# Kernel tuning notes

Hardware: AMD Instinct MI355X
Metric: run time of the kernel (lower is better)

Reference implementation:

```python
import jax, jax.numpy as jnp
import numpy as np

DEPTH = 6
IN_DIM = 768
NODE_HIDDEN = 16
LEAF_HIDDEN = 128
OUT_DIM = 768
BATCH = 4096
N_NODES = 2 ** DEPTH - 1   # 63 gating MLPs (heap/BFS order, root first)
N_LEAVES = 2 ** DEPTH      # 64 leaf MLPs


def setup_inputs() -> dict:
    key = jax.random.key(0)
    ks = jax.random.split(key, 5)
    def winit(k, shape, fan_in):
        return jax.random.normal(k, shape, jnp.float32) * (1.0 / np.sqrt(fan_in))
    return {
        "x": jax.random.normal(ks[0], (BATCH, IN_DIM), jnp.float32),
        "node_w1": winit(ks[1], (N_NODES, IN_DIM, NODE_HIDDEN), IN_DIM),
        "node_b1": jnp.zeros((N_NODES, NODE_HIDDEN), jnp.float32),
        "node_w2": winit(ks[2], (N_NODES, NODE_HIDDEN, 1), NODE_HIDDEN),
        "node_b2": jnp.zeros((N_NODES, 1), jnp.float32),
        "leaf_w1": winit(ks[3], (N_LEAVES, IN_DIM, LEAF_HIDDEN), IN_DIM),
        "leaf_b1": jnp.zeros((N_LEAVES, LEAF_HIDDEN), jnp.float32),
        "leaf_w2": winit(ks[4], (N_LEAVES, LEAF_HIDDEN, OUT_DIM), LEAF_HIDDEN),
        "leaf_b2": jnp.zeros((N_LEAVES, OUT_DIM), jnp.float32),
    }


def reference(x, node_w1, node_b1, node_w2, node_b2,
              leaf_w1, leaf_b1, leaf_w2, leaf_b2):
    """Training-mode (soft-gating) FFF tree, fully batched over all nodes/leaves.

    Equivalent to the recursive torch forward with training=True and the
    stochastic output-swap disabled (swap is a training-noise trick).
    """
    B = x.shape[0]
    # All node gates in one pass: c[b, n] = sigmoid(W2 @ relu(W1 @ x + b1) + b2)
    hn = jax.nn.relu(jnp.einsum('bi,nih->bnh', x, node_w1) + node_b1)
    c = jax.nn.sigmoid(jnp.einsum('bnh,nho->bno', hn, node_w2) + node_b2)[..., 0]  # [B, N_NODES]
    # All leaf MLPs in one pass (identity out activation)
    hl = jax.nn.relu(jnp.einsum('bi,lih->blh', x, leaf_w1) + leaf_b1)             # [B, L, LEAF_HIDDEN]
    y = jnp.einsum('blh,lho->blo', hl, leaf_w2) + leaf_b2                         # [B, L, OUT]
    # Leaf mixture weights: product of c (left) / (1-c) (right) along root->leaf path.
    # Heap index idx has children 2*idx, 2*idx+1; gate c weights the LEFT child.
    w = jnp.ones((B, 1), x.dtype)
    for lvl in range(DEPTH):
        g = c[:, 2 ** lvl - 1: 2 ** (lvl + 1) - 1]        # gates at this level, [B, 2^lvl]
        w = jnp.stack([w * g, w * (1.0 - g)], axis=-1).reshape(B, 2 ** (lvl + 1))
    return jnp.einsum('bl,blo->bo', w, y)                 # [B, OUT]
```

## Files before the change

kernel.cpp:

```cpp
#include <hip/hip_runtime.h>
#include <stdint.h>
#include <stddef.h>

typedef __attribute__((ext_vector_type(8))) short short8;
typedef __attribute__((ext_vector_type(4))) float f32x4;
typedef __attribute__((ext_vector_type(4))) short short4v;

__device__ __forceinline__ short f2bf(float f) {
  unsigned u = __builtin_bit_cast(unsigned, f);
  u = (u + 0x7fffu + ((u >> 16) & 1u)) >> 16;
  return (short)u;
}

__device__ __forceinline__ void gload16(const void* g, void* l) {
  __builtin_amdgcn_global_load_lds(
      (const __attribute__((address_space(1))) unsigned int*)g,
      (__attribute__((address_space(3))) unsigned int*)l, 16, 0, 0);
}


__global__ __launch_bounds__(256)
void cvt_misc_k(const float* __restrict__ x, const float* __restrict__ nw1,
                const float* __restrict__ lb2, short* __restrict__ xb,
                short* __restrict__ BTn, short* __restrict__ BT2) {
  const int bx = blockIdx.x;
  if (bx < 3072) {
    const int i = bx * 256 + threadIdx.x;
    const float4 v = ((const float4*)x)[i];
    short4v o;
    o.x = f2bf(v.x); o.y = f2bf(v.y); o.z = f2bf(v.z); o.w = f2bf(v.w);
    *(short4v*)(xb + (size_t)i * 4) = o;
  } else if (bx < 6144) {
    const int idx = (bx - 3072) * 256 + threadIdx.x;
    const int i = idx % 768;
    const int nh = idx / 768;
    float v = 0.f;
    if (nh < 1008) v = nw1[((size_t)(nh >> 4) * 768 + i) * 16 + (nh & 15)];
    BTn[idx] = f2bf(v);
  } else {
    const int idx = (bx - 6144) * 256 + threadIdx.x;
    const int o = idx >> 6, l = idx & 63;
    BT2[(size_t)o * 8256 + 8192 + l] = f2bf(lb2[(size_t)l * 768 + o]);
  }
}

__global__ __launch_bounds__(256, 4)
void node_cvt_k(const short* __restrict__ xb, const short* __restrict__ BTn,
                float* __restrict__ hn, const float* __restrict__ lw1,
                const float* __restrict__ lw2, short* __restrict__ BT1,
                short* __restrict__ BT2) {
  __shared__ char sh[24576];
  const int tid = threadIdx.x;
  if (blockIdx.x < 512) {
    constexpr int ABYTES = 64 * 128;
    const int lane = tid & 63, wid = tid >> 6;
    const int wm = wid >> 1, wn = wid & 1;
    const int sid = (blockIdx.x & 7) * 64 + (blockIdx.x >> 3);
    const int xg = sid % 8, yg = sid / 8;
    const int m0 = yg * 64, n0 = xg * 128;
    f32x4 acc[2][4];
    const f32x4 zero = {0.f, 0.f, 0.f, 0.f};
#pragma unroll
    for (int i = 0; i < 2; ++i)
#pragma unroll
      for (int j = 0; j < 4; ++j) acc[i][j] = zero;
    for (int ki = 0; ki < 12; ++ki) {
      const int k0 = ki * 64;
      __syncthreads();
#pragma unroll
      for (int s = 0; s < 6; ++s) {
        const int off = s * 4096 + tid * 16;
        const short* src;
        if (off < ABYTES) {
          const int r = off >> 7;
          const int cs = ((off >> 4) & 7) ^ (r & 7);
          src = xb + (size_t)(m0 + r) * 768 + k0 + cs * 8;
        } else {
          const int o2 = off - ABYTES;
          const int r = o2 >> 7;
          const int cs = ((o2 >> 4) & 7) ^ (r & 7);
          src = BTn + (size_t)(n0 + r) * 768 + k0 + cs * 8;
        }
        gload16(src, sh + off);
      }
      __syncthreads();
#pragma unroll
      for (int kk = 0; kk < 2; ++kk) {
        const int chunk = kk * 4 + (lane >> 4);
        short8 af[2], bfr[4];
#pragma unroll
        for (int i = 0; i < 2; ++i) {
          const int row = wm * 32 + i * 16 + (lane & 15);
          af[i] = *(const short8*)(sh + row * 128 + ((chunk ^ (row & 7)) << 4));
        }
#pragma unroll
        for (int j = 0; j < 4; ++j) {
          const int row = wn * 64 + j * 16 + (lane & 15);
          bfr[j] = *(const short8*)(sh + ABYTES + row * 128 + ((chunk ^ (row & 7)) << 4));
        }
#pragma unroll
        for (int i = 0; i < 2; ++i)
#pragma unroll
          for (int j = 0; j < 4; ++j)
            acc[i][j] = __builtin_amdgcn_mfma_f32_16x16x32_bf16(af[i], bfr[j], acc[i][j], 0, 0, 0);
      }
    }
    const int row_base = m0 + wm * 32 + (lane >> 4) * 4;
    const int col_base = n0 + wn * 64 + (lane & 15);
#pragma unroll
    for (int i = 0; i < 2; ++i)
#pragma unroll
      for (int j = 0; j < 4; ++j)
#pragma unroll
        for (int r = 0; r < 4; ++r)
          hn[(size_t)(row_base + i * 16 + r) * 1024 + col_base + j * 16] = acc[i][j][r];
  } else {
    float (*tile)[65] = (float(*)[65])sh;
    const int cb = blockIdx.x - 512;
    const int z = cb / 24, rem = cb % 24;
    const int by = rem / 12, bxx = rem % 12;
    const int h0 = by * 64, i0 = bxx * 64;
    if (z < 64) {
      const int l = z;
#pragma unroll
      for (int t = 0; t < 16; ++t) {
        const int e = t * 256 + tid;
        const int ii = e >> 6, hh = e & 63;
        tile[ii][hh] = lw1[(size_t)l * 98304 + (size_t)(i0 + ii) * 128 + (h0 + hh)];
      }
      __syncthreads();
#pragma unroll
      for (int t = 0; t < 16; ++t) {
        const int e = t * 256 + tid;
        const int hh = e >> 6, ii = e & 63;
        BT1[(size_t)(l * 128 + h0 + hh) * 768 + i0 + ii] = f2bf(tile[ii][hh]);
      }
    } else {
      const int l = z - 64;
      const int o0 = i0;
#pragma unroll
      for (int t = 0; t < 16; ++t) {
        const int e = t * 256 + tid;
        const int hh = e >> 6, oo = e & 63;
        tile[hh][oo] = lw2[(size_t)l * 98304 + (size_t)(h0 + hh) * 768 + (o0 + oo)];
      }
      __syncthreads();
#pragma unroll
      for (int t = 0; t < 16; ++t) {
        const int e = t * 256 + tid;
        const int oo = e >> 6, hh = e & 63;
        BT2[(size_t)(o0 + oo) * 8256 + l * 128 + h0 + hh] = f2bf(tile[hh][oo]);
      }
    }
  }
}

__global__ __launch_bounds__(256)
void gates_k(const float* __restrict__ hn, const float* __restrict__ nb1,
             const float* __restrict__ nw2, const float* __restrict__ nb2,
             float* __restrict__ wgt, short* __restrict__ hs) {
  const int b = blockIdx.x * 4 + (threadIdx.x >> 6);
  const int lane = threadIdx.x & 63;
  float c = 0.f;
  if (lane < 63) {
    float s = nb2[lane];
    const float* h = hn + (size_t)b * 1024 + lane * 16;
#pragma unroll
    for (int j = 0; j < 16; ++j) {
      float v = fmaxf(h[j] + nb1[lane * 16 + j], 0.f);
      s += v * nw2[lane * 16 + j];
    }
    c = 1.f / (1.f + expf(-s));
  }
  float w = 1.f;
#pragma unroll
  for (int lvl = 0; lvl < 6; ++lvl) {
    const int idx = (1 << lvl) - 1 + (lane >> (6 - lvl));
    const float g = __shfl(c, idx, 64);
    w *= ((lane >> (5 - lvl)) & 1) ? (1.f - g) : g;
  }
  wgt[(size_t)b * 64 + lane] = w;
  hs[(size_t)b * 8256 + 8192 + lane] = f2bf(w);
}

template <int EPI>
__global__ __launch_bounds__(512, 2)
void gemm8x(const short* __restrict__ A, const short* __restrict__ B,
            void* __restrict__ C0, float* __restrict__ P1, float* __restrict__ P2,
            float* __restrict__ P3, const float* __restrict__ bias,
            const float* __restrict__ wgt) {
  constexpr int LDA = EPI ? 768 : 8256;
  constexpr int LDB = EPI ? 768 : 8256;
  constexpr int LDC = EPI ? 8256 : 768;
  constexpr int ABYTES = 256 * 128;
  constexpr int TILEB = 2 * ABYTES;
  __shared__ char lds[2 * TILEB];

  const int tid = threadIdx.x, lane = tid & 63, wid = tid >> 6;
  const int wm = wid >> 2, wn = wid & 3;

  const int c = blockIdx.x & 7, ii = blockIdx.x >> 3;
  int xg, yg, kt0, ktn, zz;
  if constexpr (EPI == 1) {
    xg = ((c & 3) << 3) + (ii & 7);
    yg = ((c >> 2) << 3) + (ii >> 3);
    kt0 = 0; ktn = 12; zz = 0;
  } else {
    xg = ii % 3;
    const int yz = c * 8 + ii / 3;
    yg = yz & 15;
    zz = yz >> 4;
    kt0 = zz * 32;
    ktn = (zz == 3) ? 33 : 32;
  }
  const int m0 = yg * 256, n0 = xg * 256;

  f32x4 acc[8][4];
  const f32x4 zero = {0.f, 0.f, 0.f, 0.f};
#pragma unroll
  for (int i = 0; i < 8; ++i)
#pragma unroll
    for (int j = 0; j < 4; ++j) acc[i][j] = zero;

  auto STG = [&](int buf, int mat, int h, int kt) {
    const int k0 = kt * 64;
    char* dst = lds + buf * TILEB + mat * ABYTES + h * 16384;
    const short* base = mat ? B : A;
    const int ld = mat ? LDB : LDA;
    const int r0 = (mat ? n0 : m0) + h * 128;
#pragma unroll
    for (int s = 0; s < 2; ++s) {
      const int off = s * 8192 + tid * 16;
      const int r = off >> 7;
      const int cs = ((off >> 4) & 7) ^ (r & 7);
      gload16(base + (size_t)(r0 + r) * ld + k0 + cs * 8, dst + off);
    }
  };

  short8 bfrag[4][2];
  auto RD_B = [&](int buf) {
    const char* bB = lds + buf * TILEB + ABYTES;
#pragma unroll
    for (int j = 0; j < 4; ++j)
#pragma unroll
      for (int kk = 0; kk < 2; ++kk) {
        const int row = wn * 64 + j * 16 + (lane & 15);
        const int chunk = kk * 4 + (lane >> 4);
        bfrag[j][kk] = *(const short8*)(bB + row * 128 + ((chunk ^ (row & 7)) << 4));
      }
  };

  auto PH = [&](int buf, int q, bool rdB, int vm, auto&& stages) {
    if (rdB) RD_B(buf);
    const char* bA = lds + buf * TILEB;
    short8 af[2][2];
#pragma unroll
    for (int i = 0; i < 2; ++i)
#pragma unroll
      for (int kk = 0; kk < 2; ++kk) {
        const int row = wm * 128 + q * 32 + i * 16 + (lane & 15);
        const int chunk = kk * 4 + (lane >> 4);
        af[i][kk] = *(const short8*)(bA + row * 128 + ((chunk ^ (row & 7)) << 4));
      }
    stages();
    if (vm == 4) asm volatile("s_waitcnt vmcnt(4)" ::: "memory");
    else if (vm == 0) asm volatile("s_waitcnt vmcnt(0)" ::: "memory");
    __builtin_amdgcn_s_barrier();
    __builtin_amdgcn_s_setprio(1);
#pragma unroll
    for (int kk = 0; kk < 2; ++kk)
#pragma unroll
      for (int i = 0; i < 2; ++i)
#pragma unroll
        for (int j = 0; j < 4; ++j)
          acc[q * 2 + i][j] =
              __builtin_amdgcn_mfma_f32_16x16x32_bf16(af[i][kk], bfrag[j][kk], acc[q * 2 + i][j], 0, 0, 0);
    __builtin_amdgcn_s_setprio(0);
    __builtin_amdgcn_s_barrier();
  };

  STG(0, 0, 0, kt0); STG(0, 0, 1, kt0); STG(0, 1, 0, kt0); STG(0, 1, 1, kt0);
  STG(1, 1, 0, kt0 + 1); STG(1, 1, 1, kt0 + 1);
  asm volatile("s_waitcnt vmcnt(4)" ::: "memory");
  __builtin_amdgcn_s_barrier();

  const int iters = ktn >> 1;
  for (int it = 0; it < iters; ++it) {
    const int t0 = it * 2;
    const bool lastp = (it == iters - 1) && !(ktn & 1);
    const bool t2 = t0 + 2 < ktn, t3 = t0 + 3 < ktn;
    PH(0, 0, true, -1, [&] { STG(1, 0, 0, kt0 + t0 + 1); });
    PH(0, 1, false, -1, [&] {
      STG(1, 0, 1, kt0 + t0 + 1);
      if (t2) STG(0, 1, 0, kt0 + t0 + 2);
    });
    PH(0, 2, false, -1, [&] { if (t2) STG(0, 1, 1, kt0 + t0 + 2); });
    PH(0, 3, false, lastp ? 0 : 4, [] {});
    PH(1, 0, true, -1, [&] { if (t2) STG(0, 0, 0, kt0 + t0 + 2); });
    PH(1, 1, false, -1, [&] { if (t2) STG(0, 0, 1, kt0 + t0 + 2); });
    PH(1, 2, false, -1, [&] { if (t3) STG(1, 1, 0, kt0 + t0 + 3); });
    PH(1, 3, false, lastp ? -1 : 4, [&] { if (t3) STG(1, 1, 1, kt0 + t0 + 3); });
  }
  if (ktn & 1) {
    asm volatile("s_waitcnt vmcnt(0)" ::: "memory");
    __builtin_amdgcn_s_barrier();
    RD_B(0);
    const char* bA = lds;
#pragma unroll
    for (int q = 0; q < 4; ++q) {
      short8 af[2][2];
#pragma unroll
      for (int i = 0; i < 2; ++i)
#pragma unroll
        for (int kk = 0; kk < 2; ++kk) {
          const int row = wm * 128 + q * 32 + i * 16 + (lane & 15);
          const int chunk = kk * 4 + (lane >> 4);
          af[i][kk] = *(const short8*)(bA + row * 128 + ((chunk ^ (row & 7)) << 4));
        }
      __builtin_amdgcn_s_setprio(1);
#pragma unroll
      for (int kk = 0; kk < 2; ++kk)
#pragma unroll
        for (int i = 0; i < 2; ++i)
#pragma unroll
          for (int j = 0; j < 4; ++j)
            acc[q * 2 + i][j] =
                __builtin_amdgcn_mfma_f32_16x16x32_bf16(af[i][kk], bfrag[j][kk], acc[q * 2 + i][j], 0, 0, 0);
      __builtin_amdgcn_s_setprio(0);
    }
  }

  if constexpr (EPI == 1) {
    short* C = (short*)C0;
#pragma unroll
    for (int mi = 0; mi < 8; ++mi) {
      const int row_base = m0 + wm * 128 + mi * 16 + (lane >> 4) * 4;
#pragma unroll
      for (int j = 0; j < 4; ++j) {
        const int col = n0 + wn * 64 + j * 16 + (lane & 15);
        const int leaf = col >> 7;
        const float b = bias[col];
#pragma unroll
        for (int r = 0; r < 4; ++r) {
          const int row = row_base + r;
          const float v = fmaxf(acc[mi][j][r] + b, 0.f) * wgt[(size_t)row * 64 + leaf];
          C[(size_t)row * LDC + col] = f2bf(v);
        }
      }
    }
  } else {
    float* C = (zz == 0) ? (float*)C0 : (zz == 1 ? P1 : (zz == 2 ? P2 : P3));
#pragma unroll
    for (int mi = 0; mi < 8; ++mi) {
      const int row_base = m0 + wm * 128 + mi * 16 + (lane >> 4) * 4;
#pragma unroll
      for (int j = 0; j < 4; ++j) {
        const int col = n0 + wn * 64 + j * 16 + (lane & 15);
#pragma unroll
        for (int r = 0; r < 4; ++r) {
          const int row = row_base + r;
          C[(size_t)row * LDC + col] = acc[mi][j][r];
        }
      }
    }
  }
}

__global__ __launch_bounds__(256)
void reduce_k(float* __restrict__ out, const float* __restrict__ p1,
              const float* __restrict__ p2, const float* __restrict__ p3) {
  const int i = blockIdx.x * 256 + threadIdx.x;
  f32x4 a = ((const f32x4*)out)[i];
  f32x4 b = ((const f32x4*)p1)[i];
  f32x4 c = ((const f32x4*)p2)[i];
  f32x4 d = ((const f32x4*)p3)[i];
  ((f32x4*)out)[i] = (a + b) + (c + d);
}


extern "C" void kernel_launch(void* const* d_in, const int* in_sizes, int n_in,
                              void* d_out, int out_size, void* d_ws, size_t ws_size,
                              hipStream_t stream) {
  const float* x   = (const float*)d_in[0];
  const float* nw1 = (const float*)d_in[1];
  const float* nb1 = (const float*)d_in[2];
  const float* nw2 = (const float*)d_in[3];
  const float* nb2 = (const float*)d_in[4];
  const float* lw1 = (const float*)d_in[5];
  const float* lb1 = (const float*)d_in[6];
  const float* lw2 = (const float*)d_in[7];
  const float* lb2 = (const float*)d_in[8];

  char* ws = (char*)d_ws;
  short* xb  = (short*)(ws + 0);
  short* BT1 = (short*)(ws + 6291456);
  short* BTn = (short*)(ws + 18874368);
  float* hn  = (float*)(ws + 20447232);
  float* wgt = (float*)(ws + 37224448);
  short* BT2 = (short*)(ws + 38273024);
  short* hs  = (short*)(ws + 50954240);
  float* p1  = (float*)(ws + 0);
  float* p2  = (float*)(ws + 12582912);
  float* p3  = (float*)(ws + 25165824);

  cvt_misc_k<<<6336, 256, 0, stream>>>(x, nw1, lb2, xb, BTn, BT2);
  node_cvt_k<<<3584, 256, 0, stream>>>(xb, BTn, hn, lw1, lw2, BT1, BT2);

  gates_k<<<1024, 256, 0, stream>>>(hn, nb1, nw2, nb2, wgt, hs);

  gemm8x<1><<<512, 512, 0, stream>>>(xb, BT1, hs, nullptr, nullptr, nullptr,
                                     lb1, wgt);

  gemm8x<0><<<192, 512, 0, stream>>>(hs, BT2, d_out, p1, p2, p3,
                                     nullptr, nullptr);

  reduce_k<<<3072, 256, 0, stream>>>((float*)d_out, p1, p2, p3);
}
```

Measured before the change: 161.1 us.

## Rebalance GEMM grids: two N-tiles per block in GEMM1, 5-way split-K in GEMM2

The first GEMM now gives each block two adjacent 256-wide N tiles, processed back to back with a mid-loop epilogue flush. This halves the grid to 256 blocks, so a 256-CU part fills in one wave with a continuous pipeline. The second GEMM moves from 4-way to 5-way split-K (240 blocks) to fill the device better, and stores two of the partials in bf16 to cut write and reduce traffic. The cost is lower precision in part of the output accumulation and more reduction partials.

```diff
diff --git a/kernel.cpp b/kernel.cpp
--- a/kernel.cpp
+++ b/kernel.cpp
@@ -10,6 +10,11 @@
   unsigned u = __builtin_bit_cast(unsigned, f);
   u = (u + 0x7fffu + ((u >> 16) & 1u)) >> 16;
   return (short)u;
+}
+
+__device__ __forceinline__ float bf2f(short s) {
+  unsigned u = ((unsigned)(unsigned short)s) << 16;
+  return __builtin_bit_cast(float, u);
 }
 
 __device__ __forceinline__ void gload16(const void* g, void* l) {
@@ -187,8 +192,8 @@
 __global__ __launch_bounds__(512, 2)
 void gemm8x(const short* __restrict__ A, const short* __restrict__ B,
             void* __restrict__ C0, float* __restrict__ P1, float* __restrict__ P2,
-            float* __restrict__ P3, const float* __restrict__ bias,
-            const float* __restrict__ wgt) {
+            short* __restrict__ Q1, short* __restrict__ Q2,
+            const float* __restrict__ bias, const float* __restrict__ wgt) {
   constexpr int LDA = EPI ? 768 : 8256;
   constexpr int LDB = EPI ? 768 : 8256;
   constexpr int LDC = EPI ? 8256 : 768;
@@ -200,20 +205,21 @@
   const int wm = wid >> 2, wn = wid & 3;
 
   const int c = blockIdx.x & 7, ii = blockIdx.x >> 3;
-  int xg, yg, kt0, ktn, zz;
+  int xg0, yg, kt0, GKT, zz;
   if constexpr (EPI == 1) {
-    xg = ((c & 3) << 3) + (ii & 7);
-    yg = ((c >> 2) << 3) + (ii >> 3);
-    kt0 = 0; ktn = 12; zz = 0;
+    xg0 = ((((c & 3) << 2) + (ii & 3)) << 1);
+    yg = ((c >> 2) << 3) + (ii >> 2);
+    kt0 = 0; GKT = 24; zz = 0;
   } else {
-    xg = ii % 3;
-    const int yz = c * 8 + ii / 3;
-    yg = yz & 15;
-    zz = yz >> 4;
-    kt0 = zz * 32;
-    ktn = (zz == 3) ? 33 : 32;
-  }
-  const int m0 = yg * 256, n0 = xg * 256;
+    const int uid = c * 30 + ii;
+    zz = uid / 48;
+    const int r = uid % 48;
+    xg0 = r % 3; yg = r / 3;
+    kt0 = zz * 26;
+    GKT = (zz == 4) ? 25 : 26;
+  }
+  const int m0 = yg * 256;
+  const int n0fix = xg0 * 256;
 
   f32x4 acc[8][4];
   const f32x4 zero = {0.f, 0.f, 0.f, 0.f};
@@ -222,12 +228,19 @@
 #pragma unroll
     for (int j = 0; j < 4; ++j) acc[i][j] = zero;
 
-  auto STG = [&](int buf, int mat, int h, int kt) {
-    const int k0 = kt * 64;
+  auto STG = [&](int buf, int mat, int h, int gk) {
+    int k0, r0;
+    if constexpr (EPI == 1) {
+      const int ktl = (gk >= 12) ? gk - 12 : gk;
+      k0 = ktl * 64;
+      r0 = (mat ? (xg0 + (gk >= 12 ? 1 : 0)) * 256 : m0) + h * 128;
+    } else {
+      k0 = (kt0 + gk) * 64;
+      r0 = (mat ? n0fix : m0) + h * 128;
+    }
     char* dst = lds + buf * TILEB + mat * ABYTES + h * 16384;
     const short* base = mat ? B : A;
     const int ld = mat ? LDB : LDA;
-    const int r0 = (mat ? n0 : m0) + h * 128;
 #pragma unroll
     for (int s = 0; s < 2; ++s) {
       const int off = s * 8192 + tid * 16;
@@ -279,29 +292,55 @@
     __builtin_amdgcn_s_barrier();
   };
 
-  STG(0, 0, 0, kt0); STG(0, 0, 1, kt0); STG(0, 1, 0, kt0); STG(0, 1, 1, kt0);
-  STG(1, 1, 0, kt0 + 1); STG(1, 1, 1, kt0 + 1);
+  auto FLUSH1 = [&](int n0t) {
+    short* C = (short*)C0;
+#pragma unroll
+    for (int mi = 0; mi < 8; ++mi) {
+      const int row_base = m0 + wm * 128 + mi * 16 + (lane >> 4) * 4;
+#pragma unroll
+      for (int j = 0; j < 4; ++j) {
+        const int col = n0t + wn * 64 + j * 16 + (lane & 15);
+        const int leaf = col >> 7;
+        const float b = bias[col];
+#pragma unroll
+        for (int r = 0; r < 4; ++r) {
+          const int row = row_base + r;
+          const float v = fmaxf(acc[mi][j][r] + b, 0.f) * wgt[(size_t)row * 64 + leaf];
+          C[(size_t)row * LDC + col] = f2bf(v);
+        }
+      }
+    }
+#pragma unroll
+    for (int i = 0; i < 8; ++i)
+#pragma unroll
+      for (int j = 0; j < 4; ++j) acc[i][j] = zero;
+  };
+
+  STG(0, 0, 0, 0); STG(0, 0, 1, 0); STG(0, 1, 0, 0); STG(0, 1, 1, 0);
+  STG(1, 1, 0, 1); STG(1, 1, 1, 1);
   asm volatile("s_waitcnt vmcnt(4)" ::: "memory");
   __builtin_amdgcn_s_barrier();
 
-  const int iters = ktn >> 1;
+  const int iters = GKT >> 1;
   for (int it = 0; it < iters; ++it) {
     const int t0 = it * 2;
-    const bool lastp = (it == iters - 1) && !(ktn & 1);
-    const bool t2 = t0 + 2 < ktn, t3 = t0 + 3 < ktn;
-    PH(0, 0, true, -1, [&] { STG(1, 0, 0, kt0 + t0 + 1); });
+    const bool s2 = t0 + 2 < GKT, s3 = t0 + 3 < GKT;
+    PH(0, 0, true, -1, [&] { STG(1, 0, 0, t0 + 1); });
     PH(0, 1, false, -1, [&] {
-      STG(1, 0, 1, kt0 + t0 + 1);
-      if (t2) STG(0, 1, 0, kt0 + t0 + 2);
+      STG(1, 0, 1, t0 + 1);
+      if (s2) STG(0, 1, 0, t0 + 2);
     });
-    PH(0, 2, false, -1, [&] { if (t2) STG(0, 1, 1, kt0 + t0 + 2); });
-    PH(0, 3, false, lastp ? 0 : 4, [] {});
-    PH(1, 0, true, -1, [&] { if (t2) STG(0, 0, 0, kt0 + t0 + 2); });
-    PH(1, 1, false, -1, [&] { if (t2) STG(0, 0, 1, kt0 + t0 + 2); });
-    PH(1, 2, false, -1, [&] { if (t3) STG(1, 1, 0, kt0 + t0 + 3); });
-    PH(1, 3, false, lastp ? -1 : 4, [&] { if (t3) STG(1, 1, 1, kt0 + t0 + 3); });
-  }
-  if (ktn & 1) {
+    PH(0, 2, false, -1, [&] { if (s2) STG(0, 1, 1, t0 + 2); });
+    PH(0, 3, false, s2 ? 4 : 0, [] {});
+    PH(1, 0, true, -1, [&] { if (s2) STG(0, 0, 0, t0 + 2); });
+    PH(1, 1, false, -1, [&] { if (s2) STG(0, 0, 1, t0 + 2); });
+    PH(1, 2, false, -1, [&] { if (s3) STG(1, 1, 0, t0 + 3); });
+    PH(1, 3, false, s2 ? 4 : -1, [&] { if (s3) STG(1, 1, 1, t0 + 3); });
+    if constexpr (EPI == 1) {
+      if (((t0 + 2) % 12) == 0) FLUSH1((xg0 + (t0 + 1) / 12) * 256);
+    }
+  }
+  if (GKT & 1) {
     asm volatile("s_waitcnt vmcnt(0)" ::: "memory");
     __builtin_amdgcn_s_barrier();
     RD_B(0);
@@ -330,36 +369,31 @@
     }
   }
 
-  if constexpr (EPI == 1) {
-    short* C = (short*)C0;
-#pragma unroll
-    for (int mi = 0; mi < 8; ++mi) {
-      const int row_base = m0 + wm * 128 + mi * 16 + (lane >> 4) * 4;
-#pragma unroll
-      for (int j = 0; j < 4; ++j) {
-        const int col = n0 + wn * 64 + j * 16 + (lane & 15);
-        const int leaf = col >> 7;
-        const float b = bias[col];
-#pragma unroll
-        for (int r = 0; r < 4; ++r) {
-          const int row = row_base + r;
-          const float v = fmaxf(acc[mi][j][r] + b, 0.f) * wgt[(size_t)row * 64 + leaf];
-          C[(size_t)row * LDC + col] = f2bf(v);
-        }
-      }
-    }
-  } else {
-    float* C = (zz == 0) ? (float*)C0 : (zz == 1 ? P1 : (zz == 2 ? P2 : P3));
-#pragma unroll
-    for (int mi = 0; mi < 8; ++mi) {
-      const int row_base = m0 + wm * 128 + mi * 16 + (lane >> 4) * 4;
-#pragma unroll
-      for (int j = 0; j < 4; ++j) {
-        const int col = n0 + wn * 64 + j * 16 + (lane & 15);
-#pragma unroll
-        for (int r = 0; r < 4; ++r) {
-          const int row = row_base + r;
-          C[(size_t)row * LDC + col] = acc[mi][j][r];
+  if constexpr (EPI == 0) {
+    if (zz <= 2) {
+      float* C = (zz == 0) ? (float*)C0 : (zz == 1 ? P1 : P2);
+#pragma unroll
+      for (int mi = 0; mi < 8; ++mi) {
+        const int row_base = m0 + wm * 128 + mi * 16 + (lane >> 4) * 4;
+#pragma unroll
+        for (int j = 0; j < 4; ++j) {
+          const int col = n0fix + wn * 64 + j * 16 + (lane & 15);
+#pragma unroll
+          for (int r = 0; r < 4; ++r)
+            C[(size_t)(row_base + r) * LDC + col] = acc[mi][j][r];
+        }
+      }
+    } else {
+      short* Q = (zz == 3) ? Q1 : Q2;
+#pragma unroll
+      for (int mi = 0; mi < 8; ++mi) {
+        const int row_base = m0 + wm * 128 + mi * 16 + (lane >> 4) * 4;
+#pragma unroll
+        for (int j = 0; j < 4; ++j) {
+          const int col = n0fix + wn * 64 + j * 16 + (lane & 15);
+#pragma unroll
+          for (int r = 0; r < 4; ++r)
+            Q[(size_t)(row_base + r) * LDC + col] = f2bf(acc[mi][j][r]);
         }
       }
     }
@@ -368,13 +402,20 @@
 
 __global__ __launch_bounds__(256)
 void reduce_k(float* __restrict__ out, const float* __restrict__ p1,
-              const float* __restrict__ p2, const float* __restrict__ p3) {
+              const float* __restrict__ p2, const short* __restrict__ q1,
+              const short* __restrict__ q2) {
   const int i = blockIdx.x * 256 + threadIdx.x;
   f32x4 a = ((const f32x4*)out)[i];
   f32x4 b = ((const f32x4*)p1)[i];
   f32x4 c = ((const f32x4*)p2)[i];
-  f32x4 d = ((const f32x4*)p3)[i];
-  ((f32x4*)out)[i] = (a + b) + (c + d);
+  const short4v s1 = ((const short4v*)q1)[i];
+  const short4v s2 = ((const short4v*)q2)[i];
+  f32x4 r;
+  r.x = (a.x + b.x) + (c.x + bf2f(s1.x) + bf2f(s2.x));
+  r.y = (a.y + b.y) + (c.y + bf2f(s1.y) + bf2f(s2.y));
+  r.z = (a.z + b.z) + (c.z + bf2f(s1.z) + bf2f(s2.z));
+  r.w = (a.w + b.w) + (c.w + bf2f(s1.w) + bf2f(s2.w));
+  ((f32x4*)out)[i] = r;
 }
 
 
@@ -401,18 +442,19 @@
   short* hs  = (short*)(ws + 50954240);
   float* p1  = (float*)(ws + 0);
   float* p2  = (float*)(ws + 12582912);
-  float* p3  = (float*)(ws + 25165824);
+  short* q1  = (short*)(ws + 25165824);
+  short* q2  = (short*)(ws + 31457280);
 
   cvt_misc_k<<<6336, 256, 0, stream>>>(x, nw1, lb2, xb, BTn, BT2);
   node_cvt_k<<<3584, 256, 0, stream>>>(xb, BTn, hn, lw1, lw2, BT1, BT2);
 
   gates_k<<<1024, 256, 0, stream>>>(hn, nb1, nw2, nb2, wgt, hs);
 
-  gemm8x<1><<<512, 512, 0, stream>>>(xb, BT1, hs, nullptr, nullptr, nullptr,
-                                     lb1, wgt);
-
-  gemm8x<0><<<192, 512, 0, stream>>>(hs, BT2, d_out, p1, p2, p3,
+  gemm8x<1><<<256, 512, 0, stream>>>(xb, BT1, hs, nullptr, nullptr, nullptr,
+                                     nullptr, lb1, wgt);
+
+  gemm8x<0><<<240, 512, 0, stream>>>(hs, BT2, d_out, p1, p2, q1, q2,
                                      nullptr, nullptr);
 
-  reduce_k<<<3072, 256, 0, stream>>>((float*)d_out, p1, p2, p3);
-}
+  reduce_k<<<3072, 256, 0, stream>>>((float*)d_out, p1, p2, q1, q2);
+}
```

Measured after the change: 189.0 us. 1.17x slower.
